# Optimization experiments

Hardware: AMD Instinct MI355X
Metric: run time of the kernel (lower is better)

Reference implementation:

```python
import jax, jax.numpy as jnp
import numpy as np

# dims: G groups, A authors/group, P posts/author, DIN token-pooled feat, DEMB sentence-BERT dim
G, A, P, DIN, DEMB, HP, HA = 16, 64, 32, 768, 384, 256, 128


def setup_inputs() -> dict:
    key = jax.random.key(0)
    ks = jax.random.split(key, 8)
    s = lambda k, shape, scale: (jax.random.normal(k, shape, jnp.float32) * scale)
    return {
        "x": jax.random.normal(ks[0], (G, A, P, DIN), jnp.float32),
        "w_embed": s(ks[1], (DIN, DEMB), 0.02),   # BERT pooled-projection stand-in
        "b_embed": jnp.zeros((DEMB,), jnp.float32),
        "k_post": s(ks[2], (DEMB, 4 * HP), 0.05),  # Keras LSTM kernel, gates [i|f|c|o]
        "r_post": s(ks[3], (HP, 4 * HP), 0.05),    # recurrent kernel
        "b_post": jnp.zeros((4 * HP,), jnp.float32),
        "k_auth": s(ks[4], (HP, 4 * HA), 0.05),
        "r_auth": s(ks[5], (HA, 4 * HA), 0.05),
        "b_auth": jnp.zeros((4 * HA,), jnp.float32),
    }


def _lstm(x, Wk, Wr, b):
    """Keras-style LSTM, returns final hidden state. x: [B,T,D] -> [B,H]."""
    B = x.shape[0]
    H = Wr.shape[0]
    # precompute input projections for all timesteps in one GEMM: [T,B,4H]
    z = jnp.einsum('btd,dh->tbh', x, Wk) + b

    def step(carry, zt):
        h, c = carry
        g = zt + h @ Wr
        i, f, gg, o = jnp.split(g, 4, axis=-1)  # Keras gate order i,f,c,o
        c = jax.nn.sigmoid(f) * c + jax.nn.sigmoid(i) * jnp.tanh(gg)
        h = jax.nn.sigmoid(o) * jnp.tanh(c)
        return (h, c), None

    h0 = jnp.zeros((B, H), x.dtype)
    (h, _), _ = jax.lax.scan(step, (h0, h0), z)
    return h


def reference(x, w_embed, b_embed, k_post, r_post, b_post, k_auth, r_auth, b_auth):
    g, a, p, _ = x.shape
    # sentence embedding per post (BERT stand-in): [G,A,P,DEMB]
    e = jnp.einsum('gapd,de->gape', x, w_embed) + b_embed
    # LSTM over posts, batched across all (group, author) pairs: [G,A,HP]
    h_post = _lstm(e.reshape(g * a, p, e.shape[-1]), k_post, r_post, b_post)
    h_post = h_post.reshape(g, a, -1)
    # LSTM over authors: [G,HA]
    return _lstm(h_post, k_auth, r_auth, b_auth)
```

## Files before the change

### kernel.cpp

```cpp
#include <hip/hip_runtime.h>
#include <cstdint>
#include <cstddef>

#define G_    16
#define A_    64
#define P_    32
#define DIN_  768
#define DEMB_ 384
#define HP_   256
#define HA_   128
#define GA_   1024
#define N1_   1024
#define N2_   512
#define TCH   16

typedef float    f32x4   __attribute__((ext_vector_type(4)));
typedef _Float16 half8_t __attribute__((ext_vector_type(8)));
typedef _Float16 half4_t __attribute__((ext_vector_type(4)));

__device__ __forceinline__ float sigmoidf_(float x) { return 1.0f / (1.0f + __expf(-x)); }
__device__ __forceinline__ float tanhf_(float x) { return 2.0f / (1.0f + __expf(-2.0f * x)) - 1.0f; }
__device__ __forceinline__ _Float16 us2h(unsigned short u) { _Float16 h; __builtin_memcpy(&h, &u, 2); return h; }
__device__ __forceinline__ unsigned short h2us(_Float16 h) { unsigned short u; __builtin_memcpy(&u, &h, 2); return u; }


__global__ __launch_bounds__(256) void k_wk(const float* __restrict__ w_embed,
                                            const float* __restrict__ k_post,
                                            float* __restrict__ Bmat) {
    int j  = blockIdx.x * 256 + threadIdx.x;
    int k0 = blockIdx.y * 4;
    float acc0 = 0.f, acc1 = 0.f, acc2 = 0.f, acc3 = 0.f;
    for (int d = 0; d < DEMB_; ++d) {
        float kp = k_post[(size_t)d * N1_ + j];
        acc0 += w_embed[(size_t)(k0 + 0) * DEMB_ + d] * kp;
        acc1 += w_embed[(size_t)(k0 + 1) * DEMB_ + d] * kp;
        acc2 += w_embed[(size_t)(k0 + 2) * DEMB_ + d] * kp;
        acc3 += w_embed[(size_t)(k0 + 3) * DEMB_ + d] * kp;
    }
    Bmat[(size_t)(k0 + 0) * N1_ + j] = acc0;
    Bmat[(size_t)(k0 + 1) * N1_ + j] = acc1;
    Bmat[(size_t)(k0 + 2) * N1_ + j] = acc2;
    Bmat[(size_t)(k0 + 3) * N1_ + j] = acc3;
}

__global__ __launch_bounds__(256) void k_bias_p(const float* __restrict__ b_embed,
                                                const float* __restrict__ k_post,
                                                const float* __restrict__ b_post,
                                                float* __restrict__ biasZp) {
    int p = blockIdx.x * 256 + threadIdx.x;
    int n = (p >> 6) * 16 + (p & 15) + 256 * ((p >> 4) & 3);
    float acc = b_post[n];
    for (int d = 0; d < DEMB_; ++d)
        acc += b_embed[d] * k_post[(size_t)d * N1_ + n];
    biasZp[p] = acc;
}

__global__ __launch_bounds__(256) void k_t16(const float* __restrict__ Bmat,
                                             _Float16* __restrict__ Bt16) {
    __shared__ float tile[64][65];
    const int tid = threadIdx.x;
    const int p0 = blockIdx.x * 64;
    const int k0 = blockIdx.y * 64;
    const int jgrp = p0 >> 6;
#pragma unroll
    for (int i = 0; i < 16; ++i) {
        int idx = i * 256 + tid;
        int pp = idx & 63, kk = idx >> 6;
        int n = jgrp * 16 + (pp & 15) + 256 * ((pp >> 4) & 3);
        tile[pp][kk] = Bmat[(size_t)(k0 + kk) * N1_ + n];
    }
    __syncthreads();
    const int pp = tid >> 2;
    const int kq = (tid & 3) * 16;
    _Float16 buf[16];
#pragma unroll
    for (int i = 0; i < 16; ++i) buf[i] = (_Float16)tile[pp][kq + i];
    _Float16* dst = &Bt16[(size_t)(p0 + pp) * DIN_ + k0 + kq];
    *(half8_t*)dst       = *(half8_t*)&buf[0];
    *(half8_t*)(dst + 8) = *(half8_t*)&buf[8];
}

__global__ __launch_bounds__(256) void k_bfrag(const float* __restrict__ r_post,
                                               _Float16* __restrict__ Bfrag) {
    int idx = blockIdx.x * 256 + threadIdx.x;
    int pt = idx >> 9;
    int kt = (idx >> 6) & 7;
    int l  = idx & 63;
    int p = pt * 16 + (l & 15);
    int n = (p >> 6) * 16 + (p & 15) + 256 * ((p >> 4) & 3);
    int kb = kt * 32 + (l >> 4) * 8;
    _Float16 buf[8];
#pragma unroll
    for (int s = 0; s < 8; ++s) buf[s] = (_Float16)r_post[(size_t)(kb + s) * N1_ + n];
    *(half8_t*)&Bfrag[(size_t)idx * 8] = *(half8_t*)buf;
}

#define ZBM 128
#define ZBN 256
#define ZBK 32
#define ZPAD 40

__global__ __launch_bounds__(512, 2) void k_zgemm(const float* __restrict__ x,
                                                  const _Float16* __restrict__ Bt16,
                                                  const float* __restrict__ biasZp,
                                                  _Float16* __restrict__ Zq, int tbase) {
    __shared__ union {
        struct { _Float16 As[ZBM][ZPAD], Bs[ZBN][ZPAD]; } S;
        _Float16 Hs[64][264];
    } u;

    const int bid = blockIdx.x;
    const int wg  = (bid & 7) * 64 + (bid >> 3);
    const int bm  = (wg & 127) * ZBM;
    const int bn  = (wg >> 7) * ZBN;
    const int tid = threadIdx.x;

    const int arow = tid >> 2, akq = (tid & 3) * 8;
    const int brow = tid >> 1, bkq = (tid & 1) * 16;
    const int lane = tid & 63, w = tid >> 6;
    const int wm = (w >> 2) * 64, wn = (w & 3) * 64;
    const int frc = lane & 15, frk = (lane >> 4) * 8;

    const int crow = bm + arow;
    const size_t xrow = (size_t)(crow >> 4) * P_ + tbase + (crow & 15);
    const float*    aptr = &x[xrow * DIN_ + akq];
    const _Float16* bptr = &Bt16[(size_t)(bn + brow) * DIN_ + bkq];

    f32x4 acc[4][4];
#pragma unroll
    for (int i = 0; i < 4; ++i)
#pragma unroll
        for (int j = 0; j < 4; ++j) acc[i][j] = (f32x4)0.0f;

    float4 a0 = *(const float4*)aptr;
    float4 a1 = *(const float4*)(aptr + 4);
    uint4  b0 = *(const uint4*)bptr;
    uint4  b1 = *(const uint4*)(bptr + 8);

    const int NK = DIN_ / ZBK;
    for (int kt = 0; kt < NK; ++kt) {
        const int kn = (kt + 1 < NK) ? (kt + 1) * ZBK : kt * ZBK;
        float4 na0 = *(const float4*)(aptr + kn);
        float4 na1 = *(const float4*)(aptr + kn + 4);
        uint4  nb0 = *(const uint4*)(bptr + kn);
        uint4  nb1 = *(const uint4*)(bptr + kn + 8);

        half8_t ahv;
        {
            float av[8] = {a0.x,a0.y,a0.z,a0.w,a1.x,a1.y,a1.z,a1.w};
#pragma unroll
            for (int i = 0; i < 8; ++i) ahv[i] = (_Float16)av[i];
        }

        __syncthreads();
        *(half8_t*)&u.S.As[arow][akq]  = ahv;
        *(uint4*)&u.S.Bs[brow][bkq]     = b0;
        *(uint4*)&u.S.Bs[brow][bkq + 8] = b1;
        __syncthreads();

        half8_t bf[4];
#pragma unroll
        for (int fn = 0; fn < 4; ++fn)
            bf[fn] = *(const half8_t*)&u.S.Bs[wn + fn * 16 + frc][frk];
#pragma unroll
        for (int fm = 0; fm < 4; ++fm) {
            half8_t aH = *(const half8_t*)&u.S.As[wm + fm * 16 + frc][frk];
#pragma unroll
            for (int fn = 0; fn < 4; ++fn)
                acc[fm][fn] = __builtin_amdgcn_mfma_f32_16x16x32_f16(aH, bf[fn], acc[fm][fn], 0, 0, 0);
        }
        a0 = na0; a1 = na1; b0 = nb0; b1 = nb1;
    }

    float bzv[4];
#pragma unroll
    for (int fn = 0; fn < 4; ++fn) bzv[fn] = biasZp[bn + wn + fn * 16 + frc];

#pragma unroll
    for (int half_ = 0; half_ < 2; ++half_) {
        __syncthreads();
        if ((w >> 2) == half_) {
#pragma unroll
            for (int fm = 0; fm < 4; ++fm)
#pragma unroll
                for (int fn = 0; fn < 4; ++fn)
#pragma unroll
                    for (int r = 0; r < 4; ++r) {
                        int rl = fm * 16 + (lane >> 4) * 4 + r;
                        int cl = wn + fn * 16 + frc;
                        int clp = ((cl >> 6) * 16 + (cl & 15)) * 4 + ((cl >> 4) & 3);
                        u.Hs[rl][clp] = (_Float16)(acc[fm][fn][r] + bzv[fn]);
                    }
        }
        __syncthreads();
#pragma unroll
        for (int i = 0; i < 4; ++i) {
            int id = i * 512 + tid;
            int r = id >> 5, cc = (id & 31) * 8;
            int crow2 = bm + half_ * 64 + r;
            size_t zrow = (size_t)(crow2 & 15) * GA_ + (crow2 >> 4);
            *(uint4*)&Zq[zrow * N1_ + bn + cc] = *(const uint4*)&u.Hs[r][cc];
        }
    }
}

__global__ __launch_bounds__(1024, 4) void k_rec(const _Float16* __restrict__ Zq,
                                                 const _Float16* __restrict__ Bfrag,
                                                 float* __restrict__ csave,
                                                 unsigned short* __restrict__ hsave,
                                                 float* __restrict__ hF32, int tbase) {
    __shared__ __align__(16) _Float16 wlds[16 * 8 * 64 * 8];
    __shared__ __align__(16) _Float16 hbuf[2][4096];

    const int tid = threadIdx.x, lane = tid & 63, wv = tid >> 6;
    const int hl = lane & 15, l4 = lane >> 4;
    const int r0 = blockIdx.x * 16;
    const int hc = wv * 16 + hl;

    half8_t wreg[16];
#pragma unroll
    for (int q = 0; q < 2; ++q)
#pragma unroll
        for (int kt = 0; kt < 8; ++kt)
            wreg[q * 8 + kt] = *(const half8_t*)&Bfrag[(((size_t)(4 * wv + q) * 8 + kt) * 64 + lane) * 8];
#pragma unroll
    for (int kt = 0; kt < 8; ++kt)
        *(half8_t*)&wlds[((wv * 8 + kt) * 64 + lane) * 8] =
            *(const half8_t*)&Bfrag[(((size_t)(4 * wv + 2) * 8 + kt) * 64 + lane) * 8];
    const _Float16* w3base = &Bfrag[((size_t)(4 * wv + 3) * 8 * 64 + lane) * 8];

    float cst[4];
    if (tbase == 0) {
#pragma unroll
        for (int i = 0; i < 4; ++i) cst[i] = 0.f;
    } else {
        f32x4 cv = *(const f32x4*)&csave[((size_t)blockIdx.x * 1024 + tid) * 4];
#pragma unroll
        for (int i = 0; i < 4; ++i) cst[i] = cv[i];
#pragma unroll
        for (int rr = 0; rr < 4; ++rr) {
            int row = l4 * 4 + rr;
            int lidx = (((hc >> 5) * 64) + (((hc & 31) >> 3) * 16 + row)) * 8 + (hc & 7);
            hbuf[0][lidx] = us2h(hsave[((size_t)(r0 + row)) * HP_ + hc]);
        }
    }
    __syncthreads();

    const _Float16* zp = &Zq[((size_t)(r0 + l4 * 4)) * N1_ + (size_t)hc * 4];
    half4_t zvN[4];
#pragma unroll
    for (int rr = 0; rr < 4; ++rr)
        zvN[rr] = *(const half4_t*)&zp[(size_t)rr * N1_];

    for (int tt = 0; tt < TCH; ++tt) {
        const int t = tbase + tt;
        const int cur = t & 1, nxt = cur ^ 1;

        half4_t zv[4];
#pragma unroll
        for (int rr = 0; rr < 4; ++rr) zv[rr] = zvN[rr];
        zp += (size_t)GA_ * N1_;
        if (tt + 1 < TCH) {
#pragma unroll
            for (int rr = 0; rr < 4; ++rr)
                zvN[rr] = *(const half4_t*)&zp[(size_t)rr * N1_];
        }

        f32x4 acc[4];
#pragma unroll
        for (int i = 0; i < 4; ++i) acc[i] = (f32x4)0.0f;

        if (t > 0) {
#pragma unroll
            for (int kt = 0; kt < 8; ++kt) {
                half8_t ah = *(const half8_t*)&hbuf[cur][(kt * 64 + lane) * 8];
                half8_t b2 = *(const half8_t*)&wlds[((wv * 8 + kt) * 64 + lane) * 8];
                half8_t w3 = *(const half8_t*)&w3base[(size_t)kt * 512];
                acc[0] = __builtin_amdgcn_mfma_f32_16x16x32_f16(ah, wreg[kt],     acc[0], 0, 0, 0);
                acc[1] = __builtin_amdgcn_mfma_f32_16x16x32_f16(ah, wreg[8 + kt], acc[1], 0, 0, 0);
                acc[2] = __builtin_amdgcn_mfma_f32_16x16x32_f16(ah, b2,           acc[2], 0, 0, 0);
                acc[3] = __builtin_amdgcn_mfma_f32_16x16x32_f16(ah, w3,           acc[3], 0, 0, 0);
            }
        }

        const bool last = (t == P_ - 1);
        const bool save = (tbase == 0) && (tt == TCH - 1);
#pragma unroll
        for (int rr = 0; rr < 4; ++rr) {
            float gi = acc[0][rr] + (float)zv[rr][0];
            float gf = acc[1][rr] + (float)zv[rr][1];
            float gg = acc[2][rr] + (float)zv[rr][2];
            float go = acc[3][rr] + (float)zv[rr][3];
            float cn = sigmoidf_(gf) * cst[rr] + sigmoidf_(gi) * tanhf_(gg);
            cst[rr] = cn;
            float hv = sigmoidf_(go) * tanhf_(cn);
            int row = l4 * 4 + rr;
            int lidx = (((hc >> 5) * 64) + (((hc & 31) >> 3) * 16 + row)) * 8 + (hc & 7);
            _Float16 hh = (_Float16)hv;
            hbuf[nxt][lidx] = hh;
            if (save) hsave[((size_t)(r0 + row)) * HP_ + hc] = h2us(hh);
            if (last) hF32[(size_t)(r0 + row) * HP_ + hc] = hv;
        }
        __syncthreads();
    }

    if (tbase == 0) {
        f32x4 cv;
#pragma unroll
        for (int i = 0; i < 4; ++i) cv[i] = cst[i];
        *(f32x4*)&csave[((size_t)blockIdx.x * 1024 + tid) * 4] = cv;
    }
}

__global__ __launch_bounds__(256) void k_zauth(const float* __restrict__ h,
                                               const float* __restrict__ k_auth,
                                               const float* __restrict__ b_auth,
                                               float* __restrict__ z_auth) {
    const int j = blockIdx.x * 256 + threadIdx.x;
    const int r0 = blockIdx.y * 4;
    float acc0 = b_auth[j], acc1 = acc0, acc2 = acc0, acc3 = acc0;
    for (int k = 0; k < HP_; ++k) {
        const float kp = k_auth[(size_t)k * N2_ + j];
        acc0 += h[(size_t)(r0 + 0) * HP_ + k] * kp;
        acc1 += h[(size_t)(r0 + 1) * HP_ + k] * kp;
        acc2 += h[(size_t)(r0 + 2) * HP_ + k] * kp;
        acc3 += h[(size_t)(r0 + 3) * HP_ + k] * kp;
    }
#pragma unroll
    for (int r = 0; r < 4; ++r) {
        const int b = r0 + r;
        const int g = b >> 6, a = b & 63;
        const float v = (r == 0) ? acc0 : (r == 1) ? acc1 : (r == 2) ? acc2 : acc3;
        z_auth[((size_t)a * G_ + g) * N2_ + j] = v;
    }
}

__global__ __launch_bounds__(1024) void k_author(const float* __restrict__ z_auth,
                                                 const float* __restrict__ r_auth,
                                                 float* __restrict__ out) {
    const int g = blockIdx.x;
    const int tid = threadIdx.x;
    const int j = tid >> 1;
    const int kh = tid & 1;

    __shared__ float hs[HA_];
    __shared__ float gs[N2_];

    float rc[64];
#pragma unroll
    for (int kk = 0; kk < 64; ++kk)
        rc[kk] = r_auth[(size_t)(kh * 64 + kk) * N2_ + j];

    float cj = 0.f;
    if (tid < HA_) hs[tid] = 0.f;
    __syncthreads();

    for (int a = 0; a < A_; ++a) {
        float acc = kh ? 0.f : z_auth[((size_t)a * G_ + g) * N2_ + j];
#pragma unroll
        for (int kk = 0; kk < 64; ++kk)
            acc += hs[kh * 64 + kk] * rc[kk];
        acc += __shfl_xor(acc, 1);
        if (!kh) gs[j] = acc;
        __syncthreads();
        if (tid < HA_) {
            const float i_ = sigmoidf_(gs[tid]);
            const float f_ = sigmoidf_(gs[tid + 128]);
            const float gg = gs[tid + 256];
            const float o_ = sigmoidf_(gs[tid + 384]);
            cj = f_ * cj + i_ * tanhf_(gg);
            hs[tid] = o_ * tanhf_(cj);
        }
        __syncthreads();
    }
    if (tid < HA_) out[(size_t)g * HA_ + tid] = hs[tid];
}

extern "C" void kernel_launch(void* const* d_in, const int* in_sizes, int n_in,
                              void* d_out, int out_size, void* d_ws, size_t ws_size,
                              hipStream_t stream) {
    const float* x       = (const float*)d_in[0];
    const float* w_embed = (const float*)d_in[1];
    const float* b_embed = (const float*)d_in[2];
    const float* k_post  = (const float*)d_in[3];
    const float* r_post  = (const float*)d_in[4];
    const float* b_post  = (const float*)d_in[5];
    const float* k_auth  = (const float*)d_in[6];
    const float* r_auth  = (const float*)d_in[7];
    const float* b_auth  = (const float*)d_in[8];
    float* out = (float*)d_out;

    char* wsb = (char*)d_ws;
    _Float16*       Zq     = (_Float16*)(wsb);
    float*          Bmat   = (float*)(wsb + (32ull << 20));
    _Float16*       Bt16   = (_Float16*)(wsb + (36ull << 20));
    _Float16*       Bfrag  = (_Float16*)(wsb + (38ull << 20));
    float*          biasZp = (float*)(wsb + (38ull << 20) + (512ull << 10));
    float*          csave  = (float*)(wsb + (39ull << 20));
    unsigned short* hsave  = (unsigned short*)(wsb + (40ull << 20));
    float*          hF32   = (float*)(wsb + (41ull << 20));
    float*          z_auth = (float*)(wsb + (42ull << 20));

    k_wk    <<<dim3(N1_ / 256, DIN_ / 4), 256, 0, stream>>>(w_embed, k_post, Bmat);
    k_bias_p<<<dim3(N1_ / 256), 256, 0, stream>>>(b_embed, k_post, b_post, biasZp);
    k_t16   <<<dim3(16, 12), 256, 0, stream>>>(Bmat, Bt16);
    k_bfrag <<<dim3(128), 256, 0, stream>>>(r_post, Bfrag);

    for (int ch = 0; ch < 2; ++ch) {
        k_zgemm<<<dim3(512), 512, 0, stream>>>(x, Bt16, biasZp, Zq, ch * TCH);
        k_rec  <<<dim3(64), 1024, 0, stream>>>(Zq, Bfrag, csave, hsave, hF32, ch * TCH);
    }

    k_zauth <<<dim3(N2_ / 256, GA_ / 4), 256, 0, stream>>>(hF32, k_auth, b_auth, z_auth);
    k_author<<<dim3(G_), 1024, 0, stream>>>(z_auth, r_auth, out);
}
```

Before: 404.9 us.

## Halve block size in recurrent kernels, hold all recurrent weights in registers

The post-LSTM recurrence kernel now runs 512 threads per block, with each wave owning two hidden-column groups. All eight weight fragments per wave stay in registers, which removes the LDS-staged and global-streamed weight fragments from the per-step inner loop. The author LSTM kernel drops from 1024 to 512 threads: each thread computes one full gate dot product with float4 LDS reads, and the next step's z is prefetched, so the shuffle-reduce goes away. This raises register pressure (64 half8 weight fragments per thread, a 128-float array in the author kernel) and halves the waves per block, which may reduce latency hiding or cause spills.

Result: slower. 579.6 us (+43.1%).

```diff
diff --git a/kernel.cpp b/kernel.cpp
--- a/kernel.cpp
+++ b/kernel.cpp
@@ -204,111 +204,115 @@
     }
 }
 
-__global__ __launch_bounds__(1024, 4) void k_rec(const _Float16* __restrict__ Zq,
-                                                 const _Float16* __restrict__ Bfrag,
-                                                 float* __restrict__ csave,
-                                                 unsigned short* __restrict__ hsave,
-                                                 float* __restrict__ hF32, int tbase) {
-    __shared__ __align__(16) _Float16 wlds[16 * 8 * 64 * 8];
+__global__ __launch_bounds__(512, 2) void k_rec(const _Float16* __restrict__ Zq,
+                                                const _Float16* __restrict__ Bfrag,
+                                                float* __restrict__ csave,
+                                                unsigned short* __restrict__ hsave,
+                                                float* __restrict__ hF32, int tbase) {
     __shared__ __align__(16) _Float16 hbuf[2][4096];
 
     const int tid = threadIdx.x, lane = tid & 63, wv = tid >> 6;
     const int hl = lane & 15, l4 = lane >> 4;
     const int r0 = blockIdx.x * 16;
-    const int hc = wv * 16 + hl;
-
-    half8_t wreg[16];
-#pragma unroll
-    for (int q = 0; q < 2; ++q)
+    const int hcg[2] = { 2 * wv * 16 + hl, (2 * wv + 1) * 16 + hl };
+
+    half8_t wr[8][8];
+#pragma unroll
+    for (int fnl = 0; fnl < 8; ++fnl) {
+        const int fn = (2 * wv + (fnl >> 2)) * 4 + (fnl & 3);
 #pragma unroll
         for (int kt = 0; kt < 8; ++kt)
-            wreg[q * 8 + kt] = *(const half8_t*)&Bfrag[(((size_t)(4 * wv + q) * 8 + kt) * 64 + lane) * 8];
-#pragma unroll
-    for (int kt = 0; kt < 8; ++kt)
-        *(half8_t*)&wlds[((wv * 8 + kt) * 64 + lane) * 8] =
-            *(const half8_t*)&Bfrag[(((size_t)(4 * wv + 2) * 8 + kt) * 64 + lane) * 8];
-    const _Float16* w3base = &Bfrag[((size_t)(4 * wv + 3) * 8 * 64 + lane) * 8];
-
-    float cst[4];
+            wr[fnl][kt] = *(const half8_t*)&Bfrag[(((size_t)fn * 8 + kt) * 64 + lane) * 8];
+    }
+
+    float cst[8];
     if (tbase == 0) {
 #pragma unroll
-        for (int i = 0; i < 4; ++i) cst[i] = 0.f;
+        for (int i = 0; i < 8; ++i) cst[i] = 0.f;
     } else {
-        f32x4 cv = *(const f32x4*)&csave[((size_t)blockIdx.x * 1024 + tid) * 4];
-#pragma unroll
-        for (int i = 0; i < 4; ++i) cst[i] = cv[i];
-#pragma unroll
-        for (int rr = 0; rr < 4; ++rr) {
-            int row = l4 * 4 + rr;
-            int lidx = (((hc >> 5) * 64) + (((hc & 31) >> 3) * 16 + row)) * 8 + (hc & 7);
-            hbuf[0][lidx] = us2h(hsave[((size_t)(r0 + row)) * HP_ + hc]);
+#pragma unroll
+        for (int i = 0; i < 8; ++i)
+            cst[i] = csave[((size_t)blockIdx.x * 512 + tid) * 8 + i];
+#pragma unroll
+        for (int jg = 0; jg < 2; ++jg) {
+            const int hc = hcg[jg];
+#pragma unroll
+            for (int rr = 0; rr < 4; ++rr) {
+                int row = l4 * 4 + rr;
+                int lidx = (((hc >> 5) * 64) + (((hc & 31) >> 3) * 16 + row)) * 8 + (hc & 7);
+                hbuf[0][lidx] = us2h(hsave[((size_t)(r0 + row)) * HP_ + hc]);
+            }
         }
     }
     __syncthreads();
 
-    const _Float16* zp = &Zq[((size_t)(r0 + l4 * 4)) * N1_ + (size_t)hc * 4];
-    half4_t zvN[4];
-#pragma unroll
-    for (int rr = 0; rr < 4; ++rr)
-        zvN[rr] = *(const half4_t*)&zp[(size_t)rr * N1_];
+    half4_t zvN[2][4];
+#pragma unroll
+    for (int jg = 0; jg < 2; ++jg)
+#pragma unroll
+        for (int rr = 0; rr < 4; ++rr)
+            zvN[jg][rr] = *(const half4_t*)&Zq[((size_t)(r0 + l4 * 4 + rr)) * N1_ + (size_t)hcg[jg] * 4];
 
     for (int tt = 0; tt < TCH; ++tt) {
         const int t = tbase + tt;
         const int cur = t & 1, nxt = cur ^ 1;
 
-        half4_t zv[4];
-#pragma unroll
-        for (int rr = 0; rr < 4; ++rr) zv[rr] = zvN[rr];
-        zp += (size_t)GA_ * N1_;
+        half4_t zv[2][4];
+#pragma unroll
+        for (int jg = 0; jg < 2; ++jg)
+#pragma unroll
+            for (int rr = 0; rr < 4; ++rr) zv[jg][rr] = zvN[jg][rr];
         if (tt + 1 < TCH) {
 #pragma unroll
-            for (int rr = 0; rr < 4; ++rr)
-                zvN[rr] = *(const half4_t*)&zp[(size_t)rr * N1_];
-        }
-
-        f32x4 acc[4];
-#pragma unroll
-        for (int i = 0; i < 4; ++i) acc[i] = (f32x4)0.0f;
+            for (int jg = 0; jg < 2; ++jg)
+#pragma unroll
+                for (int rr = 0; rr < 4; ++rr)
+                    zvN[jg][rr] = *(const half4_t*)&Zq[((size_t)(tt + 1) * GA_ + r0 + l4 * 4 + rr) * N1_ + (size_t)hcg[jg] * 4];
+        }
+
+        f32x4 acc[8];
+#pragma unroll
+        for (int i = 0; i < 8; ++i) acc[i] = (f32x4)0.0f;
 
         if (t > 0) {
 #pragma unroll
             for (int kt = 0; kt < 8; ++kt) {
                 half8_t ah = *(const half8_t*)&hbuf[cur][(kt * 64 + lane) * 8];
-                half8_t b2 = *(const half8_t*)&wlds[((wv * 8 + kt) * 64 + lane) * 8];
-                half8_t w3 = *(const half8_t*)&w3base[(size_t)kt * 512];
-                acc[0] = __builtin_amdgcn_mfma_f32_16x16x32_f16(ah, wreg[kt],     acc[0], 0, 0, 0);
-                acc[1] = __builtin_amdgcn_mfma_f32_16x16x32_f16(ah, wreg[8 + kt], acc[1], 0, 0, 0);
-                acc[2] = __builtin_amdgcn_mfma_f32_16x16x32_f16(ah, b2,           acc[2], 0, 0, 0);
-                acc[3] = __builtin_amdgcn_mfma_f32_16x16x32_f16(ah, w3,           acc[3], 0, 0, 0);
+#pragma unroll
+                for (int fnl = 0; fnl < 8; ++fnl)
+                    acc[fnl] = __builtin_amdgcn_mfma_f32_16x16x32_f16(ah, wr[fnl][kt], acc[fnl], 0, 0, 0);
             }
         }
 
         const bool last = (t == P_ - 1);
         const bool save = (tbase == 0) && (tt == TCH - 1);
 #pragma unroll
-        for (int rr = 0; rr < 4; ++rr) {
-            float gi = acc[0][rr] + (float)zv[rr][0];
-            float gf = acc[1][rr] + (float)zv[rr][1];
-            float gg = acc[2][rr] + (float)zv[rr][2];
-            float go = acc[3][rr] + (float)zv[rr][3];
-            float cn = sigmoidf_(gf) * cst[rr] + sigmoidf_(gi) * tanhf_(gg);
-            cst[rr] = cn;
-            float hv = sigmoidf_(go) * tanhf_(cn);
-            int row = l4 * 4 + rr;
-            int lidx = (((hc >> 5) * 64) + (((hc & 31) >> 3) * 16 + row)) * 8 + (hc & 7);
-            _Float16 hh = (_Float16)hv;
-            hbuf[nxt][lidx] = hh;
-            if (save) hsave[((size_t)(r0 + row)) * HP_ + hc] = h2us(hh);
-            if (last) hF32[(size_t)(r0 + row) * HP_ + hc] = hv;
+        for (int jg = 0; jg < 2; ++jg) {
+            const int hc = hcg[jg];
+#pragma unroll
+            for (int rr = 0; rr < 4; ++rr) {
+                float gi = acc[jg * 4 + 0][rr] + (float)zv[jg][rr][0];
+                float gf = acc[jg * 4 + 1][rr] + (float)zv[jg][rr][1];
+                float gg = acc[jg * 4 + 2][rr] + (float)zv[jg][rr][2];
+                float go = acc[jg * 4 + 3][rr] + (float)zv[jg][rr][3];
+                float cn = sigmoidf_(gf) * cst[jg * 4 + rr] + sigmoidf_(gi) * tanhf_(gg);
+                cst[jg * 4 + rr] = cn;
+                float hv = sigmoidf_(go) * tanhf_(cn);
+                int row = l4 * 4 + rr;
+                int lidx = (((hc >> 5) * 64) + (((hc & 31) >> 3) * 16 + row)) * 8 + (hc & 7);
+                _Float16 hh = (_Float16)hv;
+                hbuf[nxt][lidx] = hh;
+                if (save) hsave[((size_t)(r0 + row)) * HP_ + hc] = h2us(hh);
+                if (last) hF32[(size_t)(r0 + row) * HP_ + hc] = hv;
+            }
         }
         __syncthreads();
     }
 
     if (tbase == 0) {
-        f32x4 cv;
-#pragma unroll
-        for (int i = 0; i < 4; ++i) cv[i] = cst[i];
-        *(f32x4*)&csave[((size_t)blockIdx.x * 1024 + tid) * 4] = cv;
+#pragma unroll
+        for (int i = 0; i < 8; ++i)
+            csave[((size_t)blockIdx.x * 512 + tid) * 8 + i] = cst[i];
     }
 }
 
@@ -335,33 +339,37 @@
     }
 }
 
-__global__ __launch_bounds__(1024) void k_author(const float* __restrict__ z_auth,
-                                                 const float* __restrict__ r_auth,
-                                                 float* __restrict__ out) {
+__global__ __launch_bounds__(512, 2) void k_author(const float* __restrict__ z_auth,
+                                                   const float* __restrict__ r_auth,
+                                                   float* __restrict__ out) {
     const int g = blockIdx.x;
     const int tid = threadIdx.x;
-    const int j = tid >> 1;
-    const int kh = tid & 1;
 
     __shared__ float hs[HA_];
     __shared__ float gs[N2_];
 
-    float rc[64];
-#pragma unroll
-    for (int kk = 0; kk < 64; ++kk)
-        rc[kk] = r_auth[(size_t)(kh * 64 + kk) * N2_ + j];
+    float rc[HA_];
+#pragma unroll
+    for (int k = 0; k < HA_; ++k)
+        rc[k] = r_auth[(size_t)k * N2_ + tid];
 
     float cj = 0.f;
     if (tid < HA_) hs[tid] = 0.f;
     __syncthreads();
 
+    float zn = z_auth[(size_t)g * N2_ + tid];
     for (int a = 0; a < A_; ++a) {
-        float acc = kh ? 0.f : z_auth[((size_t)a * G_ + g) * N2_ + j];
-#pragma unroll
-        for (int kk = 0; kk < 64; ++kk)
-            acc += hs[kh * 64 + kk] * rc[kk];
-        acc += __shfl_xor(acc, 1);
-        if (!kh) gs[j] = acc;
+        float acc0 = zn, acc1 = 0.f, acc2 = 0.f, acc3 = 0.f;
+        if (a + 1 < A_) zn = z_auth[((size_t)(a + 1) * G_ + g) * N2_ + tid];
+#pragma unroll
+        for (int k = 0; k < HA_; k += 4) {
+            float4 h4 = *(const float4*)&hs[k];
+            acc0 += h4.x * rc[k];
+            acc1 += h4.y * rc[k + 1];
+            acc2 += h4.z * rc[k + 2];
+            acc3 += h4.w * rc[k + 3];
+        }
+        gs[tid] = (acc0 + acc1) + (acc2 + acc3);
         __syncthreads();
         if (tid < HA_) {
             const float i_ = sigmoidf_(gs[tid]);
@@ -408,9 +416,9 @@
 
     for (int ch = 0; ch < 2; ++ch) {
         k_zgemm<<<dim3(512), 512, 0, stream>>>(x, Bt16, biasZp, Zq, ch * TCH);
-        k_rec  <<<dim3(64), 1024, 0, stream>>>(Zq, Bfrag, csave, hsave, hF32, ch * TCH);
+        k_rec  <<<dim3(64), 512, 0, stream>>>(Zq, Bfrag, csave, hsave, hF32, ch * TCH);
     }
 
     k_zauth <<<dim3(N2_ / 256, GA_ / 4), 256, 0, stream>>>(hF32, k_auth, b_auth, z_auth);
-    k_author<<<dim3(G_), 1024, 0, stream>>>(z_auth, r_auth, out);
-}
+    k_author<<<dim3(G_), 512, 0, stream>>>(z_auth, r_auth, out);
+}
```
